# Kernel optimization log

Hardware: AMD Instinct MI355X
Metric: run time of the kernel (lower is better)

## Reference

```python
import jax, jax.numpy as jnp
import numpy as np

C = 256
HEADS = 8
HD = C // HEADS
SCALE = HD ** -0.5


def conv1x1(x, W, b):
    # x: [B,C_in,H,W], W: [C_out,C_in], b: [C_out]
    return jnp.einsum('oc,bchw->bohw', W, x) + b[None, :, None, None]


def setup_inputs() -> dict:
    key = jax.random.key(0)
    ks = jax.random.split(key, 12)
    B, H, Wd = 2, 48, 48
    s = C ** -0.5
    return {
        'x': jax.random.normal(ks[0], (B, C, H, Wd), jnp.float32),
        'uncertainty': jax.random.uniform(ks[1], (B, 1, H, Wd), jnp.float32),
        'Wq': jax.random.normal(ks[2], (C, C), jnp.float32) * s,
        'bq': jnp.zeros((C,), jnp.float32),
        'Wk': jax.random.normal(ks[3], (C, C), jnp.float32) * s,
        'bk': jnp.zeros((C,), jnp.float32),
        'Wv': jax.random.normal(ks[4], (C, C), jnp.float32) * s,
        'bv': jnp.zeros((C,), jnp.float32),
        'Wg': jax.random.normal(ks[5], (C, 1), jnp.float32),
        'bg': jnp.zeros((C,), jnp.float32),
        'Wo': jax.random.normal(ks[6], (C, C), jnp.float32) * s,
        'bo': jnp.zeros((C,), jnp.float32),
    }


def reference(x, uncertainty, Wq, bq, Wk, bk, Wv, bv, Wg, bg, Wo, bo):
    B, _, H, Wd = x.shape
    N = H * Wd
    # uncertainty gate (1x1 conv from 1 channel to C channels)
    uw = conv1x1(uncertainty, Wg, bg)            # [B,C,H,W]
    gated_x = x * (1.0 - uw)
    q = conv1x1(gated_x, Wq, bq).reshape(B, HEADS, HD, N)
    k = conv1x1(gated_x, Wk, bk).reshape(B, HEADS, HD, N)
    v = conv1x1(x, Wv, bv).reshape(B, HEADS, HD, N)
    # scores: [B,h,N,N] (query tokens n, key tokens m)
    scores = jnp.einsum('bhdn,bhdm->bhnm', q, k) * SCALE
    u_flat = uncertainty.reshape(B, 1, 1, N)      # mask over key axis
    scores = scores * (1.0 - u_flat)
    attn = jax.nn.softmax(scores, axis=-1)
    out = jnp.einsum('bhnm,bhdm->bhdn', attn, v)  # [B,h,hd,N]
    out = out.reshape(B, C, H, Wd)
    out = conv1x1(out, Wo, bo)
    return out + x
```

## Files before the change

kernel.cpp:

```cpp
#include <hip/hip_runtime.h>
#include <hip/hip_bf16.h>

typedef float f32x4 __attribute__((ext_vector_type(4)));
typedef __bf16 bf16x8 __attribute__((ext_vector_type(8)));
typedef __bf16 bf16x4 __attribute__((ext_vector_type(4)));

constexpr int C = 256;
constexpr int N = 2304;
constexpr int T = 2 * N;

#if __has_builtin(__builtin_amdgcn_exp2f)
#define EXP2F(x) __builtin_amdgcn_exp2f(x)
#else
#define EXP2F(x) exp2f(x)
#endif

__device__ __forceinline__ bf16x8 load_bf8(const __bf16* p) {
    return *reinterpret_cast<const bf16x8*>(p);
}

__global__ void wconv_kernel(const float* __restrict__ Wq, const float* __restrict__ Wk,
                             const float* __restrict__ Wv, const float* __restrict__ Wo,
                             __bf16* __restrict__ Wb) {
    const float* srcs[4] = {Wq, Wk, Wv, Wo};
    int m = blockIdx.x >> 6;
    int idx = (blockIdx.x & 63) * 256 + threadIdx.x;
    float4 v = reinterpret_cast<const float4*>(srcs[m])[idx];
    bf16x4 o = { (__bf16)v.x, (__bf16)v.y, (__bf16)v.z, (__bf16)v.w };
    reinterpret_cast<bf16x4*>(Wb + m * 65536)[idx] = o;
}

__global__ void prep_kernel(const float* __restrict__ x, const float* __restrict__ u,
                            const float* __restrict__ Wg, const float* __restrict__ bg,
                            __bf16* __restrict__ xT, __bf16* __restrict__ gxT) {
    __shared__ float tile[64][65];
    int b = blockIdx.z, c0 = blockIdx.y * 64, n0 = blockIdx.x * 64;
    int t = threadIdx.x;
    const float* xp = x + (b * C + c0) * N + n0;
    #pragma unroll
    for (int r = 0; r < 16; ++r) {
        int cl = r * 4 + (t >> 6);
        int nl = t & 63;
        tile[cl][nl] = xp[cl * N + nl];
    }
    __syncthreads();
    int cq = (t & 15) * 4;
    #pragma unroll
    for (int it = 0; it < 4; ++it) {
        int nl = it * 16 + (t >> 4);
        float uv = u[b * N + n0 + nl];
        bf16x4 xo, go;
        #pragma unroll
        for (int j = 0; j < 4; ++j) {
            int c = c0 + cq + j;
            float xv = tile[cq + j][nl];
            float gate = 1.0f - (Wg[c] * uv + bg[c]);
            xo[j] = (__bf16)xv;
            go[j] = (__bf16)(xv * gate);
        }
        int tok = b * N + n0 + nl;
        *reinterpret_cast<bf16x4*>(xT + (long)tok * C + c0 + cq) = xo;
        *reinterpret_cast<bf16x4*>(gxT + (long)tok * C + c0 + cq) = go;
    }
}

__global__ __launch_bounds__(256) void qkv_kernel(const __bf16* __restrict__ Wb,
    const __bf16* __restrict__ xT, const __bf16* __restrict__ gxT,
    const float* __restrict__ bq, const float* __restrict__ bk, const float* __restrict__ bv,
    const float* __restrict__ u,
    __bf16* __restrict__ Q, __bf16* __restrict__ K, __bf16* __restrict__ V) {
    int proj = blockIdx.z;
    int o0 = blockIdx.y * 64;
    int t0 = blockIdx.x * 32;
    int wave = threadIdx.x >> 6, lane = threadIdx.x & 63;
    int g = lane >> 4, r = lane & 15;
    int ow = o0 + wave * 16;
    const __bf16* W = Wb + proj * 65536;
    const __bf16* inp = (proj == 2) ? xT : gxT;
    f32x4 acc[2] = {};
    for (int k = 0; k < 8; ++k) {
        bf16x8 a = load_bf8(W + (ow + r) * C + k * 32 + g * 8);
        #pragma unroll
        for (int tb = 0; tb < 2; ++tb) {
            bf16x8 bfr = load_bf8(inp + (long)(t0 + tb * 16 + r) * C + k * 32 + g * 8);
            acc[tb] = __builtin_amdgcn_mfma_f32_16x16x32_bf16(a, bfr, acc[tb], 0, 0, 0);
        }
    }
    const float* bias = (proj == 0) ? bq : (proj == 1) ? bk : bv;
    float bvw[4];
    #pragma unroll
    for (int i = 0; i < 4; ++i) bvw[i] = bias[ow + g * 4 + i];
    int h = ow >> 5, d0 = (ow & 31) + g * 4;
    const float SC = 0.17677669529663687f * 1.4426950408889634f;
    #pragma unroll
    for (int tb = 0; tb < 2; ++tb) {
        int t = t0 + tb * 16 + r;
        int b = t / N, n = t % N;
        if (proj == 2) {
            #pragma unroll
            for (int i = 0; i < 4; ++i)
                V[((long)(b * 8 + h) * 32 + d0 + i) * N + n] = (__bf16)(acc[tb][i] + bvw[i]);
        } else {
            bf16x4 outv;
            if (proj == 1) {
                float scale = SC * (1.0f - u[t]);
                #pragma unroll
                for (int i = 0; i < 4; ++i) outv[i] = (__bf16)((acc[tb][i] + bvw[i]) * scale);
            } else {
                #pragma unroll
                for (int i = 0; i < 4; ++i) outv[i] = (__bf16)(acc[tb][i] + bvw[i]);
            }
            __bf16* dst = (proj == 0) ? Q : K;
            *reinterpret_cast<bf16x4*>(dst + ((long)(b * 8 + h) * N + n) * 32 + d0) = outv;
        }
    }
}

__global__ __launch_bounds__(256) void attn_kernel(const __bf16* __restrict__ Q,
    const __bf16* __restrict__ K, const __bf16* __restrict__ V,
    __bf16* __restrict__ aoT) {
    __shared__ __bf16 plds[4][2][1024];
    __shared__ float po[4][2][16][32];
    __shared__ float lds_l[4][2][16];
    int id = blockIdx.x;
    int rest = id >> 3;
    int qc = rest % 72;
    int bh = (id & 7) + 8 * (rest / 72);
    int wave = threadIdx.x >> 6, lane = threadIdx.x & 63;
    int g = lane >> 4, r = lane & 15;
    int q0 = qc * 32;
    const __bf16* Qb = Q + (long)bh * N * 32;
    const __bf16* Kb = K + (long)bh * N * 32;
    const __bf16* Vb = V + (long)bh * 32 * N;
    bf16x8 qf0 = load_bf8(Qb + (q0 + r) * 32 + g * 8);
    bf16x8 qf1 = load_bf8(Qb + (q0 + 16 + r) * 32 + g * 8);
    int mbase = wave * 576;
    bf16x8 kc0 = load_bf8(Kb + (mbase +  0 + r) * 32 + g * 8);
    bf16x8 kc1 = load_bf8(Kb + (mbase + 16 + r) * 32 + g * 8);
    bf16x8 kc2 = load_bf8(Kb + (mbase + 32 + r) * 32 + g * 8);
    bf16x8 kc3 = load_bf8(Kb + (mbase + 48 + r) * 32 + g * 8);
    f32x4 oa00 = {}, oa01 = {}, oa10 = {}, oa11 = {};
    float lr0 = 0.0f, lr1 = 0.0f;
    __bf16* pl0 = plds[wave][0];
    __bf16* pl1 = plds[wave][1];
    int swz = (r & 7) << 4;
    for (int it = 0; it < 9; ++it) {
        int m0 = mbase + it * 64;
        int mp = (it == 8) ? m0 : m0 + 64;
        bf16x8 vf00 = load_bf8(Vb + (     r) * N + m0      + g * 8);
        bf16x8 vf01 = load_bf8(Vb + (16 + r) * N + m0      + g * 8);
        bf16x8 vf10 = load_bf8(Vb + (     r) * N + m0 + 32 + g * 8);
        bf16x8 vf11 = load_bf8(Vb + (16 + r) * N + m0 + 32 + g * 8);
        bf16x8 kn0 = load_bf8(Kb + (mp +  0 + r) * 32 + g * 8);
        bf16x8 kn1 = load_bf8(Kb + (mp + 16 + r) * 32 + g * 8);
        bf16x8 kn2 = load_bf8(Kb + (mp + 32 + r) * 32 + g * 8);
        bf16x8 kn3 = load_bf8(Kb + (mp + 48 + r) * 32 + g * 8);
        f32x4 z = {};
        {
            f32x4 s0 = __builtin_amdgcn_mfma_f32_16x16x32_bf16(kc0, qf0, z, 0, 0, 0);
            f32x4 s1 = __builtin_amdgcn_mfma_f32_16x16x32_bf16(kc1, qf0, z, 0, 0, 0);
            f32x4 s2 = __builtin_amdgcn_mfma_f32_16x16x32_bf16(kc2, qf0, z, 0, 0, 0);
            f32x4 s3 = __builtin_amdgcn_mfma_f32_16x16x32_bf16(kc3, qf0, z, 0, 0, 0);
            f32x4 sv[4] = {s0, s1, s2, s3};
            #pragma unroll
            for (int t = 0; t < 4; ++t) {
                bf16x4 pv;
                #pragma unroll
                for (int i = 0; i < 4; ++i) {
                    float p = EXP2F(sv[t][i]);
                    lr0 += p;
                    pv[i] = (__bf16)p;
                }
                int off = r * 128 + ((t * 32 + g * 8) ^ swz);
                *reinterpret_cast<bf16x4*>(reinterpret_cast<char*>(pl0) + off) = pv;
            }
        }
        {
            f32x4 s0 = __builtin_amdgcn_mfma_f32_16x16x32_bf16(kc0, qf1, z, 0, 0, 0);
            f32x4 s1 = __builtin_amdgcn_mfma_f32_16x16x32_bf16(kc1, qf1, z, 0, 0, 0);
            f32x4 s2 = __builtin_amdgcn_mfma_f32_16x16x32_bf16(kc2, qf1, z, 0, 0, 0);
            f32x4 s3 = __builtin_amdgcn_mfma_f32_16x16x32_bf16(kc3, qf1, z, 0, 0, 0);
            f32x4 sv[4] = {s0, s1, s2, s3};
            #pragma unroll
            for (int t = 0; t < 4; ++t) {
                bf16x4 pv;
                #pragma unroll
                for (int i = 0; i < 4; ++i) {
                    float p = EXP2F(sv[t][i]);
                    lr1 += p;
                    pv[i] = (__bf16)p;
                }
                int off = r * 128 + ((t * 32 + g * 8) ^ swz);
                *reinterpret_cast<bf16x4*>(reinterpret_cast<char*>(pl1) + off) = pv;
            }
        }
        asm volatile("s_waitcnt lgkmcnt(0)" ::: "memory");
        #pragma unroll
        for (int ch = 0; ch < 2; ++ch) {
            int off = r * 128 + ((ch * 64 + g * 16) ^ swz);
            bf16x8 pf0 = *reinterpret_cast<const bf16x8*>(reinterpret_cast<char*>(pl0) + off);
            bf16x8 pf1 = *reinterpret_cast<const bf16x8*>(reinterpret_cast<char*>(pl1) + off);
            bf16x8 v0 = ch ? vf10 : vf00;
            bf16x8 v1 = ch ? vf11 : vf01;
            oa00 = __builtin_amdgcn_mfma_f32_16x16x32_bf16(v0, pf0, oa00, 0, 0, 0);
            oa01 = __builtin_amdgcn_mfma_f32_16x16x32_bf16(v1, pf0, oa01, 0, 0, 0);
            oa10 = __builtin_amdgcn_mfma_f32_16x16x32_bf16(v0, pf1, oa10, 0, 0, 0);
            oa11 = __builtin_amdgcn_mfma_f32_16x16x32_bf16(v1, pf1, oa11, 0, 0, 0);
        }
        asm volatile("" ::: "memory");
        kc0 = kn0; kc1 = kn1; kc2 = kn2; kc3 = kn3;
    }
    float lt0 = lr0;
    lt0 += __shfl_xor(lt0, 16, 64);
    lt0 += __shfl_xor(lt0, 32, 64);
    float lt1 = lr1;
    lt1 += __shfl_xor(lt1, 16, 64);
    lt1 += __shfl_xor(lt1, 32, 64);
    *reinterpret_cast<f32x4*>(&po[wave][0][r][g * 4])      = oa00;
    *reinterpret_cast<f32x4*>(&po[wave][0][r][16 + g * 4]) = oa01;
    *reinterpret_cast<f32x4*>(&po[wave][1][r][g * 4])      = oa10;
    *reinterpret_cast<f32x4*>(&po[wave][1][r][16 + g * 4]) = oa11;
    if (g == 0) {
        lds_l[wave][0][r] = lt0;
        lds_l[wave][1][r] = lt1;
    }
    __syncthreads();
    int tid = threadIdx.x;
    int d4 = (tid & 7) * 4;
    int qi = tid >> 3;
    int qt = qi >> 4, qq = qi & 15;
    f32x4 sum = *reinterpret_cast<f32x4*>(&po[0][qt][qq][d4]);
    float l = lds_l[0][qt][qq];
    #pragma unroll
    for (int w = 1; w < 4; ++w) {
        sum += *reinterpret_cast<f32x4*>(&po[w][qt][qq][d4]);
        l += lds_l[w][qt][qq];
    }
    float inv = 1.0f / l;
    bf16x4 ov;
    #pragma unroll
    for (int i = 0; i < 4; ++i) ov[i] = (__bf16)(sum[i] * inv);
    int b = bh >> 3, h = bh & 7;
    *reinterpret_cast<bf16x4*>(aoT + (long)(b * N + q0 + qt * 16 + qq) * C + h * 32 + d4) = ov;
}

__global__ __launch_bounds__(256) void outp_kernel(const __bf16* __restrict__ Wb,
    const __bf16* __restrict__ aoT, const float* __restrict__ bo,
    const float* __restrict__ x, float* __restrict__ out) {
    int o0 = blockIdx.y * 64;
    int t0 = blockIdx.x * 32;
    int wave = threadIdx.x >> 6, lane = threadIdx.x & 63;
    int g = lane >> 4, r = lane & 15;
    int ow = o0 + wave * 16;
    const __bf16* W = Wb + 3 * 65536;
    f32x4 acc[2] = {};
    for (int k = 0; k < 8; ++k) {
        bf16x8 a = load_bf8(W + (ow + r) * C + k * 32 + g * 8);
        #pragma unroll
        for (int tb = 0; tb < 2; ++tb) {
            bf16x8 bfr = load_bf8(aoT + (long)(t0 + tb * 16 + r) * C + k * 32 + g * 8);
            acc[tb] = __builtin_amdgcn_mfma_f32_16x16x32_bf16(a, bfr, acc[tb], 0, 0, 0);
        }
    }
    float bvw[4];
    #pragma unroll
    for (int i = 0; i < 4; ++i) bvw[i] = bo[ow + g * 4 + i];
    #pragma unroll
    for (int tb = 0; tb < 2; ++tb) {
        int t = t0 + tb * 16 + r;
        int b = t / N, n = t % N;
        #pragma unroll
        for (int i = 0; i < 4; ++i) {
            long idx = ((long)b * C + ow + g * 4 + i) * N + n;
            out[idx] = acc[tb][i] + bvw[i] + x[idx];
        }
    }
}

extern "C" void kernel_launch(void* const* d_in, const int* in_sizes, int n_in,
                              void* d_out, int out_size, void* d_ws, size_t ws_size,
                              hipStream_t stream) {
    const float* x  = (const float*)d_in[0];
    const float* u  = (const float*)d_in[1];
    const float* Wq = (const float*)d_in[2];
    const float* bq = (const float*)d_in[3];
    const float* Wk = (const float*)d_in[4];
    const float* bk = (const float*)d_in[5];
    const float* Wv = (const float*)d_in[6];
    const float* bv = (const float*)d_in[7];
    const float* Wg = (const float*)d_in[8];
    const float* bg = (const float*)d_in[9];
    const float* Wo = (const float*)d_in[10];
    const float* bo = (const float*)d_in[11];
    float* out = (float*)d_out;

    char* ws = (char*)d_ws;
    size_t off = 0;
    auto alloc = [&](size_t bytes) {
        char* p = ws + off;
        off += (bytes + 255) & ~(size_t)255;
        return p;
    };
    __bf16* Wb  = (__bf16*)alloc((size_t)4 * 65536 * 2);
    __bf16* xT  = (__bf16*)alloc((size_t)T * C * 2);
    __bf16* gxT = (__bf16*)alloc((size_t)T * C * 2);
    __bf16* Qb  = (__bf16*)alloc((size_t)16 * N * 32 * 2);
    __bf16* Kb  = (__bf16*)alloc((size_t)16 * N * 32 * 2);
    __bf16* Vb  = (__bf16*)alloc((size_t)16 * N * 32 * 2);
    __bf16* aoT = (__bf16*)alloc((size_t)T * C * 2);

    wconv_kernel<<<256, 256, 0, stream>>>(Wq, Wk, Wv, Wo, Wb);
    prep_kernel<<<dim3(36, 4, 2), 256, 0, stream>>>(x, u, Wg, bg, xT, gxT);
    qkv_kernel<<<dim3(144, 4, 3), 256, 0, stream>>>(Wb, xT, gxT, bq, bk, bv, u, Qb, Kb, Vb);
    attn_kernel<<<1152, 256, 0, stream>>>(Qb, Kb, Vb, aoT);
    outp_kernel<<<dim3(144, 4), 256, 0, stream>>>(Wb, aoT, bo, x, out);
}
```

Baseline: 80.96 us.

## Feed softmax probabilities to PV MFMA directly from registers, dropping LDS staging

The attention kernel no longer writes exponentiated scores to shared memory and reads them back in a transposed layout. It uses the 16x16x16 bf16 MFMA, whose B-operand layout matches the QK^T accumulator output, so P stays in registers, and V is loaded as 4-element fragments to match. This removes LDS traffic and the lgkmcnt wait, at the cost of twice as many smaller MFMA instructions and narrower V loads.

```diff
diff --git a/kernel.cpp b/kernel.cpp
--- a/kernel.cpp
+++ b/kernel.cpp
@@ -4,6 +4,7 @@
 typedef float f32x4 __attribute__((ext_vector_type(4)));
 typedef __bf16 bf16x8 __attribute__((ext_vector_type(8)));
 typedef __bf16 bf16x4 __attribute__((ext_vector_type(4)));
+typedef short s16x4 __attribute__((ext_vector_type(4)));
 
 constexpr int C = 256;
 constexpr int N = 2304;
@@ -18,6 +19,24 @@
 __device__ __forceinline__ bf16x8 load_bf8(const __bf16* p) {
     return *reinterpret_cast<const bf16x8*>(p);
 }
+
+__device__ __forceinline__ f32x4 mfma32(bf16x8 a, bf16x8 b, f32x4 c) {
+    return __builtin_amdgcn_mfma_f32_16x16x32_bf16(a, b, c, 0, 0, 0);
+}
+
+#if __has_builtin(__builtin_amdgcn_mfma_f32_16x16x16bf16_1k)
+__device__ __forceinline__ f32x4 mfma16(bf16x4 a, bf16x4 b, f32x4 c) {
+    return __builtin_amdgcn_mfma_f32_16x16x16bf16_1k(
+        __builtin_bit_cast(s16x4, a), __builtin_bit_cast(s16x4, b), c, 0, 0, 0);
+}
+#else
+__device__ __forceinline__ f32x4 mfma16(bf16x4 a, bf16x4 b, f32x4 c) {
+    f32x4 d;
+    asm volatile("v_mfma_f32_16x16x16_bf16 %0, %1, %2, %3"
+                 : "=v"(d) : "v"(a), "v"(b), "v"(c));
+    return d;
+}
+#endif
 
 __global__ void wconv_kernel(const float* __restrict__ Wq, const float* __restrict__ Wk,
                              const float* __restrict__ Wv, const float* __restrict__ Wo,
@@ -83,7 +102,7 @@
         #pragma unroll
         for (int tb = 0; tb < 2; ++tb) {
             bf16x8 bfr = load_bf8(inp + (long)(t0 + tb * 16 + r) * C + k * 32 + g * 8);
-            acc[tb] = __builtin_amdgcn_mfma_f32_16x16x32_bf16(a, bfr, acc[tb], 0, 0, 0);
+            acc[tb] = mfma32(a, bfr, acc[tb]);
         }
     }
     const float* bias = (proj == 0) ? bq : (proj == 1) ? bk : bv;
@@ -119,7 +138,6 @@
 __global__ __launch_bounds__(256) void attn_kernel(const __bf16* __restrict__ Q,
     const __bf16* __restrict__ K, const __bf16* __restrict__ V,
     __bf16* __restrict__ aoT) {
-    __shared__ __bf16 plds[4][2][1024];
     __shared__ float po[4][2][16][32];
     __shared__ float lds_l[4][2][16];
     int id = blockIdx.x;
@@ -135,80 +153,61 @@
     bf16x8 qf0 = load_bf8(Qb + (q0 + r) * 32 + g * 8);
     bf16x8 qf1 = load_bf8(Qb + (q0 + 16 + r) * 32 + g * 8);
     int mbase = wave * 576;
-    bf16x8 kc0 = load_bf8(Kb + (mbase +  0 + r) * 32 + g * 8);
-    bf16x8 kc1 = load_bf8(Kb + (mbase + 16 + r) * 32 + g * 8);
-    bf16x8 kc2 = load_bf8(Kb + (mbase + 32 + r) * 32 + g * 8);
-    bf16x8 kc3 = load_bf8(Kb + (mbase + 48 + r) * 32 + g * 8);
+    bf16x8 kc[4];
+    #pragma unroll
+    for (int t = 0; t < 4; ++t) kc[t] = load_bf8(Kb + (mbase + t * 16 + r) * 32 + g * 8);
     f32x4 oa00 = {}, oa01 = {}, oa10 = {}, oa11 = {};
     float lr0 = 0.0f, lr1 = 0.0f;
-    __bf16* pl0 = plds[wave][0];
-    __bf16* pl1 = plds[wave][1];
-    int swz = (r & 7) << 4;
     for (int it = 0; it < 9; ++it) {
         int m0 = mbase + it * 64;
         int mp = (it == 8) ? m0 : m0 + 64;
-        bf16x8 vf00 = load_bf8(Vb + (     r) * N + m0      + g * 8);
-        bf16x8 vf01 = load_bf8(Vb + (16 + r) * N + m0      + g * 8);
-        bf16x8 vf10 = load_bf8(Vb + (     r) * N + m0 + 32 + g * 8);
-        bf16x8 vf11 = load_bf8(Vb + (16 + r) * N + m0 + 32 + g * 8);
-        bf16x8 kn0 = load_bf8(Kb + (mp +  0 + r) * 32 + g * 8);
-        bf16x8 kn1 = load_bf8(Kb + (mp + 16 + r) * 32 + g * 8);
-        bf16x8 kn2 = load_bf8(Kb + (mp + 32 + r) * 32 + g * 8);
-        bf16x8 kn3 = load_bf8(Kb + (mp + 48 + r) * 32 + g * 8);
+        bf16x4 vf[4][2];
+        #pragma unroll
+        for (int t = 0; t < 4; ++t)
+            #pragma unroll
+            for (int dt = 0; dt < 2; ++dt)
+                vf[t][dt] = *reinterpret_cast<const bf16x4*>(Vb + (dt * 16 + r) * N + m0 + t * 16 + g * 4);
+        bf16x8 kn[4];
+        #pragma unroll
+        for (int t = 0; t < 4; ++t) kn[t] = load_bf8(Kb + (mp + t * 16 + r) * 32 + g * 8);
         f32x4 z = {};
-        {
-            f32x4 s0 = __builtin_amdgcn_mfma_f32_16x16x32_bf16(kc0, qf0, z, 0, 0, 0);
-            f32x4 s1 = __builtin_amdgcn_mfma_f32_16x16x32_bf16(kc1, qf0, z, 0, 0, 0);
-            f32x4 s2 = __builtin_amdgcn_mfma_f32_16x16x32_bf16(kc2, qf0, z, 0, 0, 0);
-            f32x4 s3 = __builtin_amdgcn_mfma_f32_16x16x32_bf16(kc3, qf0, z, 0, 0, 0);
-            f32x4 sv[4] = {s0, s1, s2, s3};
+        f32x4 s0[4], s1[4];
+        #pragma unroll
+        for (int t = 0; t < 4; ++t) s0[t] = mfma32(kc[t], qf0, z);
+        #pragma unroll
+        for (int t = 0; t < 4; ++t) s1[t] = mfma32(kc[t], qf1, z);
+        bf16x4 pa0[4];
+        #pragma unroll
+        for (int t = 0; t < 4; ++t) {
             #pragma unroll
-            for (int t = 0; t < 4; ++t) {
-                bf16x4 pv;
-                #pragma unroll
-                for (int i = 0; i < 4; ++i) {
-                    float p = EXP2F(sv[t][i]);
-                    lr0 += p;
-                    pv[i] = (__bf16)p;
-                }
-                int off = r * 128 + ((t * 32 + g * 8) ^ swz);
-                *reinterpret_cast<bf16x4*>(reinterpret_cast<char*>(pl0) + off) = pv;
+            for (int i = 0; i < 4; ++i) {
+                float p = EXP2F(s0[t][i]);
+                lr0 += p;
+                pa0[t][i] = (__bf16)p;
             }
         }
-        {
-            f32x4 s0 = __builtin_amdgcn_mfma_f32_16x16x32_bf16(kc0, qf1, z, 0, 0, 0);
-            f32x4 s1 = __builtin_amdgcn_mfma_f32_16x16x32_bf16(kc1, qf1, z, 0, 0, 0);
-            f32x4 s2 = __builtin_amdgcn_mfma_f32_16x16x32_bf16(kc2, qf1, z, 0, 0, 0);
-            f32x4 s3 = __builtin_amdgcn_mfma_f32_16x16x32_bf16(kc3, qf1, z, 0, 0, 0);
-            f32x4 sv[4] = {s0, s1, s2, s3};
+        #pragma unroll
+        for (int t = 0; t < 4; ++t) {
+            oa00 = mfma16(vf[t][0], pa0[t], oa00);
+            oa01 = mfma16(vf[t][1], pa0[t], oa01);
+        }
+        bf16x4 pa1[4];
+        #pragma unroll
+        for (int t = 0; t < 4; ++t) {
             #pragma unroll
-            for (int t = 0; t < 4; ++t) {
-                bf16x4 pv;
-                #pragma unroll
-                for (int i = 0; i < 4; ++i) {
-                    float p = EXP2F(sv[t][i]);
-                    lr1 += p;
-                    pv[i] = (__bf16)p;
-                }
-                int off = r * 128 + ((t * 32 + g * 8) ^ swz);
-                *reinterpret_cast<bf16x4*>(reinterpret_cast<char*>(pl1) + off) = pv;
+            for (int i = 0; i < 4; ++i) {
+                float p = EXP2F(s1[t][i]);
+                lr1 += p;
+                pa1[t][i] = (__bf16)p;
             }
         }
-        asm volatile("s_waitcnt lgkmcnt(0)" ::: "memory");
-        #pragma unroll
-        for (int ch = 0; ch < 2; ++ch) {
-            int off = r * 128 + ((ch * 64 + g * 16) ^ swz);
-            bf16x8 pf0 = *reinterpret_cast<const bf16x8*>(reinterpret_cast<char*>(pl0) + off);
-            bf16x8 pf1 = *reinterpret_cast<const bf16x8*>(reinterpret_cast<char*>(pl1) + off);
-            bf16x8 v0 = ch ? vf10 : vf00;
-            bf16x8 v1 = ch ? vf11 : vf01;
-            oa00 = __builtin_amdgcn_mfma_f32_16x16x32_bf16(v0, pf0, oa00, 0, 0, 0);
-            oa01 = __builtin_amdgcn_mfma_f32_16x16x32_bf16(v1, pf0, oa01, 0, 0, 0);
-            oa10 = __builtin_amdgcn_mfma_f32_16x16x32_bf16(v0, pf1, oa10, 0, 0, 0);
-            oa11 = __builtin_amdgcn_mfma_f32_16x16x32_bf16(v1, pf1, oa11, 0, 0, 0);
-        }
-        asm volatile("" ::: "memory");
-        kc0 = kn0; kc1 = kn1; kc2 = kn2; kc3 = kn3;
+        #pragma unroll
+        for (int t = 0; t < 4; ++t) {
+            oa10 = mfma16(vf[t][0], pa1[t], oa10);
+            oa11 = mfma16(vf[t][1], pa1[t], oa11);
+        }
+        #pragma unroll
+        for (int t = 0; t < 4; ++t) kc[t] = kn[t];
     }
     float lt0 = lr0;
     lt0 += __shfl_xor(lt0, 16, 64);
@@ -259,7 +258,7 @@
         #pragma unroll
         for (int tb = 0; tb < 2; ++tb) {
             bf16x8 bfr = load_bf8(aoT + (long)(t0 + tb * 16 + r) * C + k * 32 + g * 8);
-            acc[tb] = __builtin_amdgcn_mfma_f32_16x16x32_bf16(a, bfr, acc[tb], 0, 0, 0);
+            acc[tb] = mfma32(a, bfr, acc[tb]);
         }
     }
     float bvw[4];
```

Measured after the change: 99.68 us. 23.1% more time.
